# Optimization experiments

Hardware: AMD Instinct MI355X
Metric: run time of the kernel (lower is better)

The kernel has to match this reference:

```python
import jax, jax.numpy as jnp
import numpy as np

NEG_SLOPE = 0.2  # PyG GATConv default leaky_relu slope
EPS = 1e-16


def layer_norm(x, g, b):
    mu = x.mean(-1, keepdims=True)
    var = ((x - mu) ** 2).mean(-1, keepdims=True)
    return (x - mu) * jax.lax.rsqrt(var + 1e-5) * g + b


def gat_conv(x, src, dst, n, W, a_src, a_dst, bias):
    # x: [N, C_in]; W: [C_in, H*C]; a_src/a_dst: [H, C]; concat=False -> mean over heads
    H, C = a_src.shape
    xh = (x @ W).reshape(n, H, C)                      # [N, H, C]
    s_src = jnp.einsum('nhc,hc->nh', xh, a_src)         # [N, H]
    s_dst = jnp.einsum('nhc,hc->nh', xh, a_dst)         # [N, H]
    e = jax.nn.leaky_relu(s_src[src] + s_dst[dst], NEG_SLOPE)  # [E, H]
    # segment softmax over incoming edges of each destination node
    m = jax.ops.segment_max(e, dst, num_segments=n)     # [N, H]
    ee = jnp.exp(e - m[dst])
    z = jax.ops.segment_sum(ee, dst, num_segments=n)    # [N, H]
    alpha = ee / (z[dst] + EPS)                         # [E, H]
    msg = xh[src] * alpha[:, :, None]                   # [E, H, C]
    out = jax.ops.segment_sum(msg, dst, num_segments=n) # [N, H, C]
    return out.mean(axis=1) + bias                      # [N, C]


def setup_inputs() -> dict:
    key = jax.random.key(0)
    N, E, C, H, L = 50000, 400000, 64, 4, 2
    ks = jax.random.split(key, 16)
    x = jax.random.normal(ks[0], (N, C), dtype=jnp.float32)
    edge_index = jax.random.randint(ks[1], (2, E), 0, N, dtype=jnp.int64)
    sc = 1.0 / np.sqrt(C)
    return {
        'x': x,
        'edge_index': edge_index,
        'Wg': jax.random.normal(ks[2], (L, C, H * C), dtype=jnp.float32) * sc,
        'att_src': jax.random.normal(ks[3], (L, H, C), dtype=jnp.float32) * sc,
        'att_dst': jax.random.normal(ks[4], (L, H, C), dtype=jnp.float32) * sc,
        'att_bias': jnp.zeros((L, C), dtype=jnp.float32),
        'ln1_g': jnp.ones((L, C), dtype=jnp.float32),
        'ln1_b': jnp.zeros((L, C), dtype=jnp.float32),
        'W1': jax.random.normal(ks[5], (L, C, C), dtype=jnp.float32) * sc,
        'b1': jnp.zeros((L, C), dtype=jnp.float32),
        'W2': jax.random.normal(ks[6], (L, C, C), dtype=jnp.float32) * sc,
        'b2': jnp.zeros((L, C), dtype=jnp.float32),
        'ln2_g': jnp.ones((L, C), dtype=jnp.float32),
        'ln2_b': jnp.zeros((L, C), dtype=jnp.float32),
    }


def reference(x, edge_index, Wg, att_src, att_dst, att_bias,
              ln1_g, ln1_b, W1, b1, W2, b2, ln2_g, ln2_b):
    n = x.shape[0]
    L = Wg.shape[0]
    # PyG GATConv adds self loops by default
    loops = jnp.arange(n, dtype=edge_index.dtype)
    src = jnp.concatenate([edge_index[0], loops])
    dst = jnp.concatenate([edge_index[1], loops])
    for i in range(L):
        x_att = gat_conv(x, src, dst, n, Wg[i], att_src[i], att_dst[i], att_bias[i])
        x = layer_norm(x + x_att, ln1_g[i], ln1_b[i])
        h = jax.nn.relu(x @ W1[i] + b1[i])
        h = h @ W2[i] + b2[i]
        x = layer_norm(x + h, ln2_g[i], ln2_b[i])
    return x
```

## Files before the change

kernel.cpp:

```cpp
#include <hip/hip_runtime.h>
#include <hip/hip_bf16.h>
#include <float.h>

#define C 64
#define H 4
#define HC 256
#define NEG_SLOPE 0.2f
#define EPS_SEG 1e-16f
#define LN_EPS 1e-5f
#define ROWB 576

typedef __attribute__((ext_vector_type(8))) short bf16x8;
typedef __attribute__((ext_vector_type(4))) float f32x4;

__device__ __forceinline__ float warp_sum(float v) {
#pragma unroll
    for (int m = 32; m >= 1; m >>= 1) v += __shfl_xor(v, m, 64);
    return v;
}

__device__ __forceinline__ unsigned short f2bf(float f) {
    unsigned int u = __float_as_uint(f);
    return (unsigned short)((u + 0x7FFF + ((u >> 16) & 1)) >> 16);
}
__device__ __forceinline__ float bf2f(unsigned short u) {
    return __uint_as_float(((unsigned int)u) << 16);
}


__global__ void k_zero(int* __restrict__ a, int n) {
    int i = blockIdx.x * blockDim.x + threadIdx.x;
    int stride = gridDim.x * blockDim.x;
    for (int j = i; j < n; j += stride) a[j] = 0;
}

__global__ void k_count(const int* __restrict__ ei, int* __restrict__ counts,
                        int E, int Etot) {
    int eid = blockIdx.x * blockDim.x + threadIdx.x;
    if (eid >= Etot) return;
    int d = (eid < E) ? ei[E + eid] : eid - E;
    atomicAdd(&counts[d], 1);
}

__global__ __launch_bounds__(256) void k_scan1(const int* __restrict__ counts,
                                               int* __restrict__ tmp,
                                               int* __restrict__ bsum, int N) {
    __shared__ int sm[256];
    int t = threadIdx.x;
    int i = blockIdx.x * 256 + t;
    sm[t] = (i < N) ? counts[i] : 0;
    __syncthreads();
    for (int off = 1; off < 256; off <<= 1) {
        int add = (t >= off) ? sm[t - off] : 0;
        __syncthreads();
        sm[t] += add;
        __syncthreads();
    }
    if (i < N) tmp[i] = sm[t];
    if (t == 255) bsum[blockIdx.x] = sm[255];
}

__global__ __launch_bounds__(256) void k_scan2(int* __restrict__ bsum, int nb) {
    __shared__ int sm[256];
    int t = threadIdx.x;
    sm[t] = (t < nb) ? bsum[t] : 0;
    __syncthreads();
    for (int off = 1; off < 256; off <<= 1) {
        int add = (t >= off) ? sm[t - off] : 0;
        __syncthreads();
        sm[t] += add;
        __syncthreads();
    }
    if (t < nb) bsum[t] = (t > 0) ? sm[t - 1] : 0;
}

__global__ __launch_bounds__(256) void k_scan3(const int* __restrict__ tmp,
                                               const int* __restrict__ boff,
                                               int* __restrict__ rowptr,
                                               int* __restrict__ cursor, int N) {
    int i = blockIdx.x * 256 + threadIdx.x;
    if (i < N) {
        rowptr[i + 1] = tmp[i] + boff[blockIdx.x];
        cursor[i] = 0;
    }
    if (i == 0) rowptr[0] = 0;
}

__global__ void k_fill(const int* __restrict__ ei, const int* __restrict__ rowptr,
                       int* __restrict__ cursor, int* __restrict__ col,
                       int E, int Etot) {
    int eid = blockIdx.x * blockDim.x + threadIdx.x;
    if (eid >= Etot) return;
    int s, d;
    if (eid < E) { s = ei[eid]; d = ei[E + eid]; } else { s = d = eid - E; }
    int pos = rowptr[d] + atomicAdd(&cursor[d], 1);
    col[pos] = s;
}


__global__ void k_prep_x(const float4* __restrict__ xin, ushort4* __restrict__ xb,
                         int n4, int npad4) {
    int i = blockIdx.x * blockDim.x + threadIdx.x;
    int st = gridDim.x * blockDim.x;
    for (int j = i; j < npad4; j += st) {
        ushort4 o;
        if (j < n4) {
            float4 v = xin[j];
            o.x = f2bf(v.x); o.y = f2bf(v.y); o.z = f2bf(v.z); o.w = f2bf(v.w);
        } else {
            o.x = o.y = o.z = o.w = 0;
        }
        xb[j] = o;
    }
}

__global__ void k_prep_weights(const float* __restrict__ Wg,
                               const float* __restrict__ W1, const float* __restrict__ W2,
                               unsigned short* __restrict__ Wgt,
                               unsigned short* __restrict__ W1t,
                               unsigned short* __restrict__ W2t, int L) {
    int i = blockIdx.x * 256 + threadIdx.x;
    int nWg = L * C * HC;
    int nW = L * C * C;
    if (i < nWg) {
        int l = i / (C * HC);
        int r = i - l * C * HC;
        int n = r >> 6, k = r & 63;
        Wgt[(size_t)l * HC * C + n * C + k] = f2bf(Wg[(size_t)l * C * HC + k * HC + n]);
    } else if (i < nWg + nW) {
        int j = i - nWg;
        int l = j / (C * C);
        int r = j - l * C * C;
        int n = r >> 6, k = r & 63;
        W1t[(size_t)l * C * C + n * C + k] = f2bf(W1[(size_t)l * C * C + k * C + n]);
        W2t[(size_t)l * C * C + n * C + k] = f2bf(W2[(size_t)l * C * C + k * C + n]);
    }
}

__global__ __launch_bounds__(256) void k_gemm_mfma(
    const unsigned short* __restrict__ xb, const unsigned short* __restrict__ Wgt,
    const float* __restrict__ a_src, const float* __restrict__ a_dst,
    char* __restrict__ xhs, float* __restrict__ s_dst, int N)
{
    int w = threadIdx.x >> 6, l = threadIdx.x & 63;
    int n0 = blockIdx.x * 64;
    int lr = l & 15, lk = (l >> 4) * 8;
    bf16x8 bfr[4][2];
    float as[4], ad[4];
#pragma unroll
    for (int ct = 0; ct < 4; ct++) {
        int colg = w * 64 + ct * 16 + lr;
#pragma unroll
        for (int ks = 0; ks < 2; ks++)
            bfr[ct][ks] = *reinterpret_cast<const bf16x8*>(Wgt + colg * C + ks * 32 + lk);
        as[ct] = a_src[w * C + ct * 16 + lr];
        ad[ct] = a_dst[w * C + ct * 16 + lr];
    }
#pragma unroll
    for (int rt = 0; rt < 4; rt++) {
        const unsigned short* arow = xb + (size_t)(n0 + rt * 16 + lr) * C + lk;
        bf16x8 a0 = *reinterpret_cast<const bf16x8*>(arow);
        bf16x8 a1 = *reinterpret_cast<const bf16x8*>(arow + 32);
        f32x4 acc[4];
#pragma unroll
        for (int ct = 0; ct < 4; ct++) {
            acc[ct] = (f32x4){0.f, 0.f, 0.f, 0.f};
            acc[ct] = __builtin_amdgcn_mfma_f32_16x16x32_bf16(a0, bfr[ct][0], acc[ct], 0, 0, 0);
            acc[ct] = __builtin_amdgcn_mfma_f32_16x16x32_bf16(a1, bfr[ct][1], acc[ct], 0, 0, 0);
        }
        int nbase = n0 + rt * 16 + (l >> 4) * 4;
#pragma unroll
        for (int ct = 0; ct < 4; ct++) {
            int cb = (w * 64 + ct * 16 + lr) * 2;
#pragma unroll
            for (int r = 0; r < 4; r++) {
                int n = nbase + r;
                if (n < N)
                    *(unsigned short*)(xhs + (size_t)n * ROWB + cb) = f2bf(acc[ct][r]);
            }
        }
#pragma unroll
        for (int r = 0; r < 4; r++) {
            float ps = acc[0][r] * as[0] + acc[1][r] * as[1]
                     + acc[2][r] * as[2] + acc[3][r] * as[3];
            float pd = acc[0][r] * ad[0] + acc[1][r] * ad[1]
                     + acc[2][r] * ad[2] + acc[3][r] * ad[3];
#pragma unroll
            for (int off = 1; off < 16; off <<= 1) {
                ps += __shfl_xor(ps, off, 64);
                pd += __shfl_xor(pd, off, 64);
            }
            int n = nbase + r;
            if (lr == 0 && n < N) {
                *(float*)(xhs + (size_t)n * ROWB + 512 + w * 4) = ps;
                s_dst[n * H + w] = pd;
            }
        }
    }
}

__global__ __launch_bounds__(256) void k_gat_node(
    const int* __restrict__ rowptr, const int* __restrict__ col,
    const float* __restrict__ s_dst, const char* __restrict__ xhs,
    const float* __restrict__ x_in, const float* __restrict__ bias,
    const float* __restrict__ g, const float* __restrict__ b,
    float* __restrict__ x1, unsigned short* __restrict__ x1b, int N)
{
    int n = (blockIdx.x * blockDim.x + threadIdx.x) >> 6;
    int l = threadIdx.x & 63;
    int h = l >> 4, gq = l & 15;
    if (n >= N) return;
    int r0 = rowptr[n], r1 = rowptr[n + 1];

    float4 xi = *(const float4*)(x_in + (size_t)n * C + gq * 4);
    float4 bia = *(const float4*)(bias + gq * 4);
    float sdh = s_dst[n * H + h];

    int laneoff = h * 128 + gq * 8;
    int ssoff = 512 + h * 4;

    float a0 = 0.f, a1 = 0.f, a2 = 0.f, a3 = 0.f, z = 0.f;

    int j = r0;
    for (; j + 4 <= r1; j += 4) {
        int s0 = col[j], s1 = col[j + 1], s2 = col[j + 2], s3 = col[j + 3];
        const char* p0 = xhs + (size_t)s0 * ROWB;
        const char* p1 = xhs + (size_t)s1 * ROWB;
        const char* p2 = xhs + (size_t)s2 * ROWB;
        const char* p3 = xhs + (size_t)s3 * ROWB;
        uint2 v0 = *(const uint2*)(p0 + laneoff);
        uint2 v1 = *(const uint2*)(p1 + laneoff);
        uint2 v2 = *(const uint2*)(p2 + laneoff);
        uint2 v3 = *(const uint2*)(p3 + laneoff);
        float e0 = *(const float*)(p0 + ssoff) + sdh;
        float e1 = *(const float*)(p1 + ssoff) + sdh;
        float e2 = *(const float*)(p2 + ssoff) + sdh;
        float e3 = *(const float*)(p3 + ssoff) + sdh;
        float w0 = __expf(fmaxf(e0, NEG_SLOPE * e0));
        float w1 = __expf(fmaxf(e1, NEG_SLOPE * e1));
        float w2 = __expf(fmaxf(e2, NEG_SLOPE * e2));
        float w3 = __expf(fmaxf(e3, NEG_SLOPE * e3));
        a0 += w0 * __uint_as_float(v0.x << 16);
        a1 += w0 * __uint_as_float(v0.x & 0xFFFF0000u);
        a2 += w0 * __uint_as_float(v0.y << 16);
        a3 += w0 * __uint_as_float(v0.y & 0xFFFF0000u);
        a0 += w1 * __uint_as_float(v1.x << 16);
        a1 += w1 * __uint_as_float(v1.x & 0xFFFF0000u);
        a2 += w1 * __uint_as_float(v1.y << 16);
        a3 += w1 * __uint_as_float(v1.y & 0xFFFF0000u);
        a0 += w2 * __uint_as_float(v2.x << 16);
        a1 += w2 * __uint_as_float(v2.x & 0xFFFF0000u);
        a2 += w2 * __uint_as_float(v2.y << 16);
        a3 += w2 * __uint_as_float(v2.y & 0xFFFF0000u);
        a0 += w3 * __uint_as_float(v3.x << 16);
        a1 += w3 * __uint_as_float(v3.x & 0xFFFF0000u);
        a2 += w3 * __uint_as_float(v3.y << 16);
        a3 += w3 * __uint_as_float(v3.y & 0xFFFF0000u);
        z += w0 + w1 + w2 + w3;
    }
    {
        int t = r1 - j;
        int s0 = 0, s1 = 0, s2 = 0;
        if (t > 0) s0 = col[j];
        if (t > 1) s1 = col[j + 1];
        if (t > 2) s2 = col[j + 2];
        const char* p0 = xhs + (size_t)s0 * ROWB;
        const char* p1 = xhs + (size_t)s1 * ROWB;
        const char* p2 = xhs + (size_t)s2 * ROWB;
        uint2 v0 = {0, 0}, v1 = {0, 0}, v2 = {0, 0};
        float e0 = 0.f, e1 = 0.f, e2 = 0.f;
        if (t > 0) { v0 = *(const uint2*)(p0 + laneoff); e0 = *(const float*)(p0 + ssoff) + sdh; }
        if (t > 1) { v1 = *(const uint2*)(p1 + laneoff); e1 = *(const float*)(p1 + ssoff) + sdh; }
        if (t > 2) { v2 = *(const uint2*)(p2 + laneoff); e2 = *(const float*)(p2 + ssoff) + sdh; }
        float w0 = (t > 0) ? __expf(fmaxf(e0, NEG_SLOPE * e0)) : 0.f;
        float w1 = (t > 1) ? __expf(fmaxf(e1, NEG_SLOPE * e1)) : 0.f;
        float w2 = (t > 2) ? __expf(fmaxf(e2, NEG_SLOPE * e2)) : 0.f;
        a0 += w0 * __uint_as_float(v0.x << 16);
        a1 += w0 * __uint_as_float(v0.x & 0xFFFF0000u);
        a2 += w0 * __uint_as_float(v0.y << 16);
        a3 += w0 * __uint_as_float(v0.y & 0xFFFF0000u);
        a0 += w1 * __uint_as_float(v1.x << 16);
        a1 += w1 * __uint_as_float(v1.x & 0xFFFF0000u);
        a2 += w1 * __uint_as_float(v1.y << 16);
        a3 += w1 * __uint_as_float(v1.y & 0xFFFF0000u);
        a0 += w2 * __uint_as_float(v2.x << 16);
        a1 += w2 * __uint_as_float(v2.x & 0xFFFF0000u);
        a2 += w2 * __uint_as_float(v2.y << 16);
        a3 += w2 * __uint_as_float(v2.y & 0xFFFF0000u);
        z += w0 + w1 + w2;
    }

    float inv = 0.25f / (z + EPS_SEG);
    a0 *= inv; a1 *= inv; a2 *= inv; a3 *= inv;
#pragma unroll
    for (int off = 16; off <= 32; off <<= 1) {
        a0 += __shfl_xor(a0, off, 64);
        a1 += __shfl_xor(a1, off, 64);
        a2 += __shfl_xor(a2, off, 64);
        a3 += __shfl_xor(a3, off, 64);
    }
    float y0 = xi.x + a0 + bia.x;
    float y1 = xi.y + a1 + bia.y;
    float y2 = xi.z + a2 + bia.z;
    float y3 = xi.w + a3 + bia.w;
    float mu = warp_sum(y0 + y1 + y2 + y3) * (1.f / (C * 4));
    float d0 = y0 - mu, d1 = y1 - mu, d2 = y2 - mu, d3 = y3 - mu;
    float var = warp_sum(d0 * d0 + d1 * d1 + d2 * d2 + d3 * d3) * (1.f / (C * 4));
    float rs = rsqrtf(var + LN_EPS);
    if (h == 0) {
        float4 gg = *(const float4*)(g + gq * 4);
        float4 bb = *(const float4*)(b + gq * 4);
        float4 o;
        o.x = d0 * rs * gg.x + bb.x;
        o.y = d1 * rs * gg.y + bb.y;
        o.z = d2 * rs * gg.z + bb.z;
        o.w = d3 * rs * gg.w + bb.w;
        *(float4*)(x1 + (size_t)n * C + gq * 4) = o;
        ushort4 ob;
        ob.x = f2bf(o.x); ob.y = f2bf(o.y); ob.z = f2bf(o.z); ob.w = f2bf(o.w);
        *(ushort4*)(x1b + (size_t)n * C + gq * 4) = ob;
    }
}

__global__ __launch_bounds__(256) void k_ffn_mfma(
    const float* __restrict__ x1f, const unsigned short* __restrict__ x1b,
    const unsigned short* __restrict__ W1t, const unsigned short* __restrict__ W2t,
    const float* __restrict__ b1, const float* __restrict__ b2,
    const float* __restrict__ g, const float* __restrict__ b,
    float* __restrict__ xout, unsigned short* __restrict__ xb, int N)
{
    __shared__ unsigned short hls[64 * 64];
    int w = threadIdx.x >> 6, l = threadIdx.x & 63;
    int lr = l & 15, q = l >> 4, lk = q * 8;
    int n0 = blockIdx.x * 64;

    {
        bf16x8 bf[4][2];
#pragma unroll
        for (int ct = 0; ct < 4; ct++)
#pragma unroll
            for (int ks = 0; ks < 2; ks++)
                bf[ct][ks] = *reinterpret_cast<const bf16x8*>(
                    W1t + (ct * 16 + lr) * C + ks * 32 + lk);
        const unsigned short* arow = x1b + (size_t)(n0 + w * 16 + lr) * C + lk;
        bf16x8 a0 = *reinterpret_cast<const bf16x8*>(arow);
        bf16x8 a1 = *reinterpret_cast<const bf16x8*>(arow + 32);
        f32x4 acc[4];
#pragma unroll
        for (int ct = 0; ct < 4; ct++) {
            acc[ct] = (f32x4){0.f, 0.f, 0.f, 0.f};
            acc[ct] = __builtin_amdgcn_mfma_f32_16x16x32_bf16(a0, bf[ct][0], acc[ct], 0, 0, 0);
            acc[ct] = __builtin_amdgcn_mfma_f32_16x16x32_bf16(a1, bf[ct][1], acc[ct], 0, 0, 0);
        }
#pragma unroll
        for (int ct = 0; ct < 4; ct++) {
            float bc = b1[ct * 16 + lr];
#pragma unroll
            for (int r = 0; r < 4; r++) {
                float v = fmaxf(acc[ct][r] + bc, 0.f);
                int rowb = w * 16 + q * 4 + r;
                int byte = rowb * 128 + (ct * 16 + lr) * 2;
                byte ^= (rowb & 7) << 4;
                *(unsigned short*)((char*)hls + byte) = f2bf(v);
            }
        }
    }
    __syncthreads();

    bf16x8 bf[4][2];
#pragma unroll
    for (int ct = 0; ct < 4; ct++)
#pragma unroll
        for (int ks = 0; ks < 2; ks++)
            bf[ct][ks] = *reinterpret_cast<const bf16x8*>(
                W2t + (ct * 16 + lr) * C + ks * 32 + lk);
    bf16x8 h0, h1;
    {
        int rowb = w * 16 + lr;
        int swz = (rowb & 7) << 4;
        int byte0 = (rowb * 128 + q * 16) ^ swz;
        int byte1 = (rowb * 128 + 64 + q * 16) ^ swz;
        h0 = *(bf16x8*)((char*)hls + byte0);
        h1 = *(bf16x8*)((char*)hls + byte1);
    }
    f32x4 acc[4];
#pragma unroll
    for (int ct = 0; ct < 4; ct++) {
        acc[ct] = (f32x4){0.f, 0.f, 0.f, 0.f};
        acc[ct] = __builtin_amdgcn_mfma_f32_16x16x32_bf16(h0, bf[ct][0], acc[ct], 0, 0, 0);
        acc[ct] = __builtin_amdgcn_mfma_f32_16x16x32_bf16(h1, bf[ct][1], acc[ct], 0, 0, 0);
    }

    float b2c[4], gc[4], bc[4];
#pragma unroll
    for (int ct = 0; ct < 4; ct++) {
        int cg = ct * 16 + lr;
        b2c[ct] = b2[cg]; gc[ct] = g[cg]; bc[ct] = b[cg];
    }
    float yv[4][4];
#pragma unroll
    for (int r = 0; r < 4; r++) {
        int n = n0 + w * 16 + q * 4 + r;
        bool ok = n < N;
#pragma unroll
        for (int ct = 0; ct < 4; ct++) {
            float xr = ok ? x1f[(size_t)n * C + ct * 16 + lr] : 0.f;
            yv[ct][r] = acc[ct][r] + b2c[ct] + xr;
        }
    }
#pragma unroll
    for (int r = 0; r < 4; r++) {
        int n = n0 + w * 16 + q * 4 + r;
        float s = yv[0][r] + yv[1][r] + yv[2][r] + yv[3][r];
#pragma unroll
        for (int off = 1; off < 16; off <<= 1) s += __shfl_xor(s, off, 64);
        float mu = s * (1.f / C);
        float d0 = yv[0][r] - mu, d1 = yv[1][r] - mu;
        float d2 = yv[2][r] - mu, d3 = yv[3][r] - mu;
        float vs = d0 * d0 + d1 * d1 + d2 * d2 + d3 * d3;
#pragma unroll
        for (int off = 1; off < 16; off <<= 1) vs += __shfl_xor(vs, off, 64);
        float rs = rsqrtf(vs * (1.f / C) + LN_EPS);
        if (n < N) {
            float dd[4] = {d0, d1, d2, d3};
#pragma unroll
            for (int ct = 0; ct < 4; ct++) {
                float o = dd[ct] * rs * gc[ct] + bc[ct];
                xout[(size_t)n * C + ct * 16 + lr] = o;
                xb[(size_t)n * C + ct * 16 + lr] = f2bf(o);
            }
        }
    }
}

extern "C" void kernel_launch(void* const* d_in, const int* in_sizes, int n_in,
                              void* d_out, int out_size, void* d_ws, size_t ws_size,
                              hipStream_t stream) {
    const float* x        = (const float*)d_in[0];
    const int*   ei       = (const int*)d_in[1];
    const float* Wg       = (const float*)d_in[2];
    const float* a_src    = (const float*)d_in[3];
    const float* a_dst    = (const float*)d_in[4];
    const float* att_bias = (const float*)d_in[5];
    const float* ln1_g    = (const float*)d_in[6];
    const float* ln1_b    = (const float*)d_in[7];
    const float* W1       = (const float*)d_in[8];
    const float* b1       = (const float*)d_in[9];
    const float* W2       = (const float*)d_in[10];
    const float* b2       = (const float*)d_in[11];
    const float* ln2_g    = (const float*)d_in[12];
    const float* ln2_b    = (const float*)d_in[13];
    float* xout = (float*)d_out;

    int N = in_sizes[0] / C;
    int E = in_sizes[1] / 2;
    int Etot = E + N;
    int L = in_sizes[2] / (C * HC);
    int nb = (N + 255) / 256;
    int Npad = (N + 63) & ~63;

    char* p = (char*)d_ws;
    auto alloc = [&](size_t bytes) { void* r = (void*)p; p += (bytes + 255) & ~(size_t)255; return r; };
    float* s_dst = (float*)alloc((size_t)N * H * 4);
    float* x1    = (float*)alloc((size_t)N * C * 4);
    int* rowptr  = (int*)alloc((size_t)(N + 1) * 4);
    int* col     = (int*)alloc((size_t)Etot * 4);
    int* counts  = (int*)alloc((size_t)N * 4);
    int* tmp     = (int*)alloc((size_t)N * 4);
    int* bsum    = (int*)alloc((size_t)nb * 4);
    unsigned short* xb  = (unsigned short*)alloc((size_t)Npad * C * 2);
    unsigned short* x1b = (unsigned short*)alloc((size_t)Npad * C * 2);
    unsigned short* Wgt = (unsigned short*)alloc((size_t)L * HC * C * 2);
    unsigned short* W1t = (unsigned short*)alloc((size_t)L * C * C * 2);
    unsigned short* W2t = (unsigned short*)alloc((size_t)L * C * C * 2);
    char* xhs = (char*)alloc((size_t)N * ROWB);

    k_zero<<<256, 256, 0, stream>>>(counts, N);
    k_count<<<(Etot + 255) / 256, 256, 0, stream>>>(ei, counts, E, Etot);
    k_scan1<<<nb, 256, 0, stream>>>(counts, tmp, bsum, N);
    k_scan2<<<1, 256, 0, stream>>>(bsum, nb);
    k_scan3<<<nb, 256, 0, stream>>>(tmp, bsum, rowptr, counts, N);
    k_fill<<<(Etot + 255) / 256, 256, 0, stream>>>(ei, rowptr, counts, col, E, Etot);
    k_prep_x<<<2048, 256, 0, stream>>>((const float4*)x, (ushort4*)xb,
                                       N * C / 4, Npad * C / 4);
    {
        int tot = L * C * HC + L * C * C;
        k_prep_weights<<<(tot + 255) / 256, 256, 0, stream>>>(Wg, W1, W2, Wgt, W1t, W2t, L);
    }

    for (int l = 0; l < L; l++) {
        const float* xin = (l == 0) ? x : xout;
        k_gemm_mfma<<<Npad / 64, 256, 0, stream>>>(
            xb, Wgt + (size_t)l * HC * C, a_src + l * H * C, a_dst + l * H * C,
            xhs, s_dst, N);
        k_gat_node<<<(N + 3) / 4, 256, 0, stream>>>(
            rowptr, col, s_dst, xhs, xin,
            att_bias + l * C, ln1_g + l * C, ln1_b + l * C, x1, x1b, N);
        k_ffn_mfma<<<Npad / 64, 256, 0, stream>>>(
            x1, x1b, W1t + (size_t)l * C * C, W2t + (size_t)l * C * C,
            b1 + l * C, b2 + l * C, ln2_g + l * C, ln2_b + l * C, xout, xb, N);
    }
}
```

Before: 218.5 us.

## Map 16 lanes per node in GAT aggregation with double-buffered neighbor loads

The GAT aggregation kernel now gives each destination node 16 lanes instead of a full 64-lane wavefront, so one wavefront serves four nodes. Each lane handles two heads and 8 channels using 16-byte loads. The neighbor loop is software-pipelined: the next neighbor's row is fetched while the current one is accumulated. The aim is to raise the number of gather loads in flight per wavefront and cut idle lanes. In exchange, the four nodes in a wavefront diverge by degree because the loop runs until all are done, and each lane uses more registers.

After: 225.3 us. 1.03x slower.

```diff
diff --git a/kernel.cpp b/kernel.cpp
--- a/kernel.cpp
+++ b/kernel.cpp
@@ -22,9 +22,6 @@
 __device__ __forceinline__ unsigned short f2bf(float f) {
     unsigned int u = __float_as_uint(f);
     return (unsigned short)((u + 0x7FFF + ((u >> 16) & 1)) >> 16);
-}
-__device__ __forceinline__ float bf2f(unsigned short u) {
-    return __uint_as_float(((unsigned int)u) << 16);
 }
 
 
@@ -206,119 +203,126 @@
     const float* __restrict__ g, const float* __restrict__ b,
     float* __restrict__ x1, unsigned short* __restrict__ x1b, int N)
 {
-    int n = (blockIdx.x * blockDim.x + threadIdx.x) >> 6;
     int l = threadIdx.x & 63;
-    int h = l >> 4, gq = l & 15;
-    if (n >= N) return;
-    int r0 = rowptr[n], r1 = rowptr[n + 1];
-
-    float4 xi = *(const float4*)(x_in + (size_t)n * C + gq * 4);
-    float4 bia = *(const float4*)(bias + gq * 4);
-    float sdh = s_dst[n * H + h];
-
-    int laneoff = h * 128 + gq * 8;
-    int ssoff = 512 + h * 4;
-
-    float a0 = 0.f, a1 = 0.f, a2 = 0.f, a3 = 0.f, z = 0.f;
-
-    int j = r0;
-    for (; j + 4 <= r1; j += 4) {
-        int s0 = col[j], s1 = col[j + 1], s2 = col[j + 2], s3 = col[j + 3];
-        const char* p0 = xhs + (size_t)s0 * ROWB;
-        const char* p1 = xhs + (size_t)s1 * ROWB;
-        const char* p2 = xhs + (size_t)s2 * ROWB;
-        const char* p3 = xhs + (size_t)s3 * ROWB;
-        uint2 v0 = *(const uint2*)(p0 + laneoff);
-        uint2 v1 = *(const uint2*)(p1 + laneoff);
-        uint2 v2 = *(const uint2*)(p2 + laneoff);
-        uint2 v3 = *(const uint2*)(p3 + laneoff);
-        float e0 = *(const float*)(p0 + ssoff) + sdh;
-        float e1 = *(const float*)(p1 + ssoff) + sdh;
-        float e2 = *(const float*)(p2 + ssoff) + sdh;
-        float e3 = *(const float*)(p3 + ssoff) + sdh;
-        float w0 = __expf(fmaxf(e0, NEG_SLOPE * e0));
-        float w1 = __expf(fmaxf(e1, NEG_SLOPE * e1));
-        float w2 = __expf(fmaxf(e2, NEG_SLOPE * e2));
-        float w3 = __expf(fmaxf(e3, NEG_SLOPE * e3));
-        a0 += w0 * __uint_as_float(v0.x << 16);
-        a1 += w0 * __uint_as_float(v0.x & 0xFFFF0000u);
-        a2 += w0 * __uint_as_float(v0.y << 16);
-        a3 += w0 * __uint_as_float(v0.y & 0xFFFF0000u);
-        a0 += w1 * __uint_as_float(v1.x << 16);
-        a1 += w1 * __uint_as_float(v1.x & 0xFFFF0000u);
-        a2 += w1 * __uint_as_float(v1.y << 16);
-        a3 += w1 * __uint_as_float(v1.y & 0xFFFF0000u);
-        a0 += w2 * __uint_as_float(v2.x << 16);
-        a1 += w2 * __uint_as_float(v2.x & 0xFFFF0000u);
-        a2 += w2 * __uint_as_float(v2.y << 16);
-        a3 += w2 * __uint_as_float(v2.y & 0xFFFF0000u);
-        a0 += w3 * __uint_as_float(v3.x << 16);
-        a1 += w3 * __uint_as_float(v3.x & 0xFFFF0000u);
-        a2 += w3 * __uint_as_float(v3.y << 16);
-        a3 += w3 * __uint_as_float(v3.y & 0xFFFF0000u);
-        z += w0 + w1 + w2 + w3;
-    }
-    {
-        int t = r1 - j;
-        int s0 = 0, s1 = 0, s2 = 0;
-        if (t > 0) s0 = col[j];
-        if (t > 1) s1 = col[j + 1];
-        if (t > 2) s2 = col[j + 2];
-        const char* p0 = xhs + (size_t)s0 * ROWB;
-        const char* p1 = xhs + (size_t)s1 * ROWB;
-        const char* p2 = xhs + (size_t)s2 * ROWB;
-        uint2 v0 = {0, 0}, v1 = {0, 0}, v2 = {0, 0};
-        float e0 = 0.f, e1 = 0.f, e2 = 0.f;
-        if (t > 0) { v0 = *(const uint2*)(p0 + laneoff); e0 = *(const float*)(p0 + ssoff) + sdh; }
-        if (t > 1) { v1 = *(const uint2*)(p1 + laneoff); e1 = *(const float*)(p1 + ssoff) + sdh; }
-        if (t > 2) { v2 = *(const uint2*)(p2 + laneoff); e2 = *(const float*)(p2 + ssoff) + sdh; }
-        float w0 = (t > 0) ? __expf(fmaxf(e0, NEG_SLOPE * e0)) : 0.f;
-        float w1 = (t > 1) ? __expf(fmaxf(e1, NEG_SLOPE * e1)) : 0.f;
-        float w2 = (t > 2) ? __expf(fmaxf(e2, NEG_SLOPE * e2)) : 0.f;
-        a0 += w0 * __uint_as_float(v0.x << 16);
-        a1 += w0 * __uint_as_float(v0.x & 0xFFFF0000u);
-        a2 += w0 * __uint_as_float(v0.y << 16);
-        a3 += w0 * __uint_as_float(v0.y & 0xFFFF0000u);
-        a0 += w1 * __uint_as_float(v1.x << 16);
-        a1 += w1 * __uint_as_float(v1.x & 0xFFFF0000u);
-        a2 += w1 * __uint_as_float(v1.y << 16);
-        a3 += w1 * __uint_as_float(v1.y & 0xFFFF0000u);
-        a0 += w2 * __uint_as_float(v2.x << 16);
-        a1 += w2 * __uint_as_float(v2.x & 0xFFFF0000u);
-        a2 += w2 * __uint_as_float(v2.y << 16);
-        a3 += w2 * __uint_as_float(v2.y & 0xFFFF0000u);
-        z += w0 + w1 + w2;
-    }
-
-    float inv = 0.25f / (z + EPS_SEG);
-    a0 *= inv; a1 *= inv; a2 *= inv; a3 *= inv;
-#pragma unroll
-    for (int off = 16; off <= 32; off <<= 1) {
-        a0 += __shfl_xor(a0, off, 64);
-        a1 += __shfl_xor(a1, off, 64);
-        a2 += __shfl_xor(a2, off, 64);
-        a3 += __shfl_xor(a3, off, 64);
-    }
-    float y0 = xi.x + a0 + bia.x;
-    float y1 = xi.y + a1 + bia.y;
-    float y2 = xi.z + a2 + bia.z;
-    float y3 = xi.w + a3 + bia.w;
-    float mu = warp_sum(y0 + y1 + y2 + y3) * (1.f / (C * 4));
-    float d0 = y0 - mu, d1 = y1 - mu, d2 = y2 - mu, d3 = y3 - mu;
-    float var = warp_sum(d0 * d0 + d1 * d1 + d2 * d2 + d3 * d3) * (1.f / (C * 4));
-    float rs = rsqrtf(var + LN_EPS);
-    if (h == 0) {
-        float4 gg = *(const float4*)(g + gq * 4);
-        float4 bb = *(const float4*)(b + gq * 4);
-        float4 o;
-        o.x = d0 * rs * gg.x + bb.x;
-        o.y = d1 * rs * gg.y + bb.y;
-        o.z = d2 * rs * gg.z + bb.z;
-        o.w = d3 * rs * gg.w + bb.w;
-        *(float4*)(x1 + (size_t)n * C + gq * 4) = o;
-        ushort4 ob;
-        ob.x = f2bf(o.x); ob.y = f2bf(o.y); ob.z = f2bf(o.z); ob.w = f2bf(o.w);
-        *(ushort4*)(x1b + (size_t)n * C + gq * 4) = ob;
+    int il = l & 15;
+    int n = blockIdx.x * 16 + ((threadIdx.x >> 6) << 2) + (l >> 4);
+    bool nvalid = n < N;
+    int nn = nvalid ? n : 0;
+    int r0 = rowptr[nn];
+    int r1 = rowptr[nn + 1];
+    int deg = nvalid ? (r1 - r0) : 0;
+
+    int hsel = (il >> 3) & 1;
+    float sdA = s_dst[nn * H + hsel];
+    float sdB = s_dst[nn * H + 2 + hsel];
+    int c0 = (il & 7) * 8;
+    int byteoff = il * 16;
+
+    float acc0[8], acc1[8];
+#pragma unroll
+    for (int k = 0; k < 8; k++) { acc0[k] = 0.f; acc1[k] = 0.f; }
+    float zA = 0.f, zB = 0.f;
+
+    uint4 a0v = {0,0,0,0}, a1v = {0,0,0,0};
+    float4 asv = {0.f,0.f,0.f,0.f};
+    bool actA = 0 < deg;
+    if (actA) {
+        const char* p = xhs + (size_t)col[r0] * ROWB;
+        a0v = *(const uint4*)(p + byteoff);
+        a1v = *(const uint4*)(p + 256 + byteoff);
+        asv = *(const float4*)(p + 512);
+    }
+
+#define GAT_COMPUTE(V0, V1, SV, ACT)                                          \
+    {                                                                         \
+        float ea = (hsel ? (SV).y : (SV).x) + sdA;                            \
+        float eb = (hsel ? (SV).w : (SV).z) + sdB;                            \
+        float wA = (ACT) ? __expf(fmaxf(ea, NEG_SLOPE * ea)) : 0.f;           \
+        float wB = (ACT) ? __expf(fmaxf(eb, NEG_SLOPE * eb)) : 0.f;           \
+        unsigned int uu0[4] = {(V0).x, (V0).y, (V0).z, (V0).w};               \
+        unsigned int uu1[4] = {(V1).x, (V1).y, (V1).z, (V1).w};               \
+        _Pragma("unroll")                                                     \
+        for (int q = 0; q < 4; q++) {                                         \
+            acc0[2*q]   += wA * __uint_as_float(uu0[q] << 16);                \
+            acc0[2*q+1] += wA * __uint_as_float(uu0[q] & 0xFFFF0000u);        \
+            acc1[2*q]   += wB * __uint_as_float(uu1[q] << 16);                \
+            acc1[2*q+1] += wB * __uint_as_float(uu1[q] & 0xFFFF0000u);        \
+        }                                                                     \
+        zA += wA; zB += wB;                                                   \
+    }
+
+    int t = 0;
+    while (__any(actA)) {
+        bool actB = (t + 1) < deg;
+        uint4 b0v = {0,0,0,0}, b1v = {0,0,0,0};
+        float4 bsv = {0.f,0.f,0.f,0.f};
+        if (actB) {
+            const char* p = xhs + (size_t)col[r0 + t + 1] * ROWB;
+            b0v = *(const uint4*)(p + byteoff);
+            b1v = *(const uint4*)(p + 256 + byteoff);
+            bsv = *(const float4*)(p + 512);
+        }
+        GAT_COMPUTE(a0v, a1v, asv, actA);
+        actA = (t + 2) < deg;
+        if (actA) {
+            const char* p = xhs + (size_t)col[r0 + t + 2] * ROWB;
+            a0v = *(const uint4*)(p + byteoff);
+            a1v = *(const uint4*)(p + 256 + byteoff);
+            asv = *(const float4*)(p + 512);
+        } else {
+            a0v = (uint4){0,0,0,0}; a1v = (uint4){0,0,0,0};
+            asv = (float4){0.f,0.f,0.f,0.f};
+        }
+        GAT_COMPUTE(b0v, b1v, bsv, actB);
+        t += 2;
+    }
+#undef GAT_COMPUTE
+
+    float izA = 1.f / (zA + EPS_SEG);
+    float izB = 1.f / (zB + EPS_SEG);
+    float y[8];
+#pragma unroll
+    for (int k = 0; k < 8; k++) {
+        float v = acc0[k] * izA + acc1[k] * izB;
+        v += __shfl_xor(v, 8, 64);
+        y[k] = v * 0.25f;
+    }
+    float xi[8], bi[8];
+    *(float4*)&xi[0] = *(const float4*)(x_in + (size_t)nn * C + c0);
+    *(float4*)&xi[4] = *(const float4*)(x_in + (size_t)nn * C + c0 + 4);
+    *(float4*)&bi[0] = *(const float4*)(bias + c0);
+    *(float4*)&bi[4] = *(const float4*)(bias + c0 + 4);
+#pragma unroll
+    for (int k = 0; k < 8; k++) y[k] += xi[k] + bi[k];
+    float s = 0.f;
+#pragma unroll
+    for (int k = 0; k < 8; k++) s += y[k];
+#pragma unroll
+    for (int off = 1; off <= 8; off <<= 1) s += __shfl_xor(s, off, 64);
+    float mu = s * (1.f / 128.f);
+    float vs = 0.f;
+    float dv[8];
+#pragma unroll
+    for (int k = 0; k < 8; k++) { dv[k] = y[k] - mu; vs += dv[k] * dv[k]; }
+#pragma unroll
+    for (int off = 1; off <= 8; off <<= 1) vs += __shfl_xor(vs, off, 64);
+    float rs = rsqrtf(vs * (1.f / 128.f) + LN_EPS);
+    if (il < 8 && nvalid) {
+        float gg[8], bb[8];
+        *(float4*)&gg[0] = *(const float4*)(g + c0);
+        *(float4*)&gg[4] = *(const float4*)(g + c0 + 4);
+        *(float4*)&bb[0] = *(const float4*)(b + c0);
+        *(float4*)&bb[4] = *(const float4*)(b + c0 + 4);
+        float o[8];
+        ushort4 ob0, ob1;
+#pragma unroll
+        for (int k = 0; k < 8; k++) o[k] = dv[k] * rs * gg[k] + bb[k];
+        *(float4*)(x1 + (size_t)n * C + c0) = *(float4*)&o[0];
+        *(float4*)(x1 + (size_t)n * C + c0 + 4) = *(float4*)&o[4];
+        ob0.x = f2bf(o[0]); ob0.y = f2bf(o[1]); ob0.z = f2bf(o[2]); ob0.w = f2bf(o[3]);
+        ob1.x = f2bf(o[4]); ob1.y = f2bf(o[5]); ob1.z = f2bf(o[6]); ob1.w = f2bf(o[7]);
+        *(ushort4*)(x1b + (size_t)n * C + c0) = ob0;
+        *(ushort4*)(x1b + (size_t)n * C + c0 + 4) = ob1;
     }
 }
 
@@ -493,7 +497,7 @@
         k_gemm_mfma<<<Npad / 64, 256, 0, stream>>>(
             xb, Wgt + (size_t)l * HC * C, a_src + l * H * C, a_dst + l * H * C,
             xhs, s_dst, N);
-        k_gat_node<<<(N + 3) / 4, 256, 0, stream>>>(
+        k_gat_node<<<(N + 15) / 16, 256, 0, stream>>>(
             rowptr, col, s_dst, xhs, xin,
             att_bias + l * C, ln1_g + l * C, ln1_b + l * C, x1, x1b, N);
         k_ffn_mfma<<<Npad / 64, 256, 0, stream>>>(
```

## Split s_src out of packed node rows and unroll edge gather by eight

Applied to the files above, without the earlier changes.

The packed per-node row that stored bf16 features plus the source attention scores (576 bytes) is split into a 512-byte feature array and a separate compact s_src array. The GAT aggregation loop is unrolled from four to eight edges per iteration, with a tail that handles up to seven remaining edges. The aim is power-of-two row strides and more outstanding gather loads per wavefront to hide latency. The cost is an extra scattered load stream for s_src per edge and higher register pressure from the wider unroll.

After: 234.3 us. 1.07x slower.

```diff
diff --git a/kernel.cpp b/kernel.cpp
--- a/kernel.cpp
+++ b/kernel.cpp
@@ -8,7 +8,6 @@
 #define NEG_SLOPE 0.2f
 #define EPS_SEG 1e-16f
 #define LN_EPS 1e-5f
-#define ROWB 576
 
 typedef __attribute__((ext_vector_type(8))) short bf16x8;
 typedef __attribute__((ext_vector_type(4))) float f32x4;
@@ -22,9 +21,6 @@
 __device__ __forceinline__ unsigned short f2bf(float f) {
     unsigned int u = __float_as_uint(f);
     return (unsigned short)((u + 0x7FFF + ((u >> 16) & 1)) >> 16);
-}
-__device__ __forceinline__ float bf2f(unsigned short u) {
-    return __uint_as_float(((unsigned int)u) << 16);
 }
 
 
@@ -140,7 +136,8 @@
 __global__ __launch_bounds__(256) void k_gemm_mfma(
     const unsigned short* __restrict__ xb, const unsigned short* __restrict__ Wgt,
     const float* __restrict__ a_src, const float* __restrict__ a_dst,
-    char* __restrict__ xhs, float* __restrict__ s_dst, int N)
+    unsigned short* __restrict__ xh, float* __restrict__ s_src,
+    float* __restrict__ s_dst, int N)
 {
     int w = threadIdx.x >> 6, l = threadIdx.x & 63;
     int n0 = blockIdx.x * 64;
@@ -171,12 +168,11 @@
         int nbase = n0 + rt * 16 + (l >> 4) * 4;
 #pragma unroll
         for (int ct = 0; ct < 4; ct++) {
-            int cb = (w * 64 + ct * 16 + lr) * 2;
+            int colg = w * 64 + ct * 16 + lr;
 #pragma unroll
             for (int r = 0; r < 4; r++) {
                 int n = nbase + r;
-                if (n < N)
-                    *(unsigned short*)(xhs + (size_t)n * ROWB + cb) = f2bf(acc[ct][r]);
+                if (n < N) xh[(size_t)n * HC + colg] = f2bf(acc[ct][r]);
             }
         }
 #pragma unroll
@@ -192,7 +188,7 @@
             }
             int n = nbase + r;
             if (lr == 0 && n < N) {
-                *(float*)(xhs + (size_t)n * ROWB + 512 + w * 4) = ps;
+                s_src[n * H + w] = ps;
                 s_dst[n * H + w] = pd;
             }
         }
@@ -201,7 +197,8 @@
 
 __global__ __launch_bounds__(256) void k_gat_node(
     const int* __restrict__ rowptr, const int* __restrict__ col,
-    const float* __restrict__ s_dst, const char* __restrict__ xhs,
+    const float* __restrict__ s_src, const float* __restrict__ s_dst,
+    const unsigned short* __restrict__ xh,
     const float* __restrict__ x_in, const float* __restrict__ bias,
     const float* __restrict__ g, const float* __restrict__ b,
     float* __restrict__ x1, unsigned short* __restrict__ x1b, int N)
@@ -216,79 +213,79 @@
     float4 bia = *(const float4*)(bias + gq * 4);
     float sdh = s_dst[n * H + h];
 
+    const char* xbase = (const char*)xh;
     int laneoff = h * 128 + gq * 8;
-    int ssoff = 512 + h * 4;
 
     float a0 = 0.f, a1 = 0.f, a2 = 0.f, a3 = 0.f, z = 0.f;
 
+#define GACC(vv, ww)                                         \
+    a0 += (ww) * __uint_as_float((vv).x << 16);              \
+    a1 += (ww) * __uint_as_float((vv).x & 0xFFFF0000u);      \
+    a2 += (ww) * __uint_as_float((vv).y << 16);              \
+    a3 += (ww) * __uint_as_float((vv).y & 0xFFFF0000u);      \
+    z += (ww);
+
     int j = r0;
-    for (; j + 4 <= r1; j += 4) {
-        int s0 = col[j], s1 = col[j + 1], s2 = col[j + 2], s3 = col[j + 3];
-        const char* p0 = xhs + (size_t)s0 * ROWB;
-        const char* p1 = xhs + (size_t)s1 * ROWB;
-        const char* p2 = xhs + (size_t)s2 * ROWB;
-        const char* p3 = xhs + (size_t)s3 * ROWB;
-        uint2 v0 = *(const uint2*)(p0 + laneoff);
-        uint2 v1 = *(const uint2*)(p1 + laneoff);
-        uint2 v2 = *(const uint2*)(p2 + laneoff);
-        uint2 v3 = *(const uint2*)(p3 + laneoff);
-        float e0 = *(const float*)(p0 + ssoff) + sdh;
-        float e1 = *(const float*)(p1 + ssoff) + sdh;
-        float e2 = *(const float*)(p2 + ssoff) + sdh;
-        float e3 = *(const float*)(p3 + ssoff) + sdh;
+    for (; j + 8 <= r1; j += 8) {
+        int s0 = col[j],     s1 = col[j + 1], s2 = col[j + 2], s3 = col[j + 3];
+        int s4 = col[j + 4], s5 = col[j + 5], s6 = col[j + 6], s7 = col[j + 7];
+        uint2 v0 = *(const uint2*)(xbase + (size_t)s0 * 512 + laneoff);
+        uint2 v1 = *(const uint2*)(xbase + (size_t)s1 * 512 + laneoff);
+        uint2 v2 = *(const uint2*)(xbase + (size_t)s2 * 512 + laneoff);
+        uint2 v3 = *(const uint2*)(xbase + (size_t)s3 * 512 + laneoff);
+        uint2 v4 = *(const uint2*)(xbase + (size_t)s4 * 512 + laneoff);
+        uint2 v5 = *(const uint2*)(xbase + (size_t)s5 * 512 + laneoff);
+        uint2 v6 = *(const uint2*)(xbase + (size_t)s6 * 512 + laneoff);
+        uint2 v7 = *(const uint2*)(xbase + (size_t)s7 * 512 + laneoff);
+        float e0 = s_src[s0 * H + h] + sdh;
+        float e1 = s_src[s1 * H + h] + sdh;
+        float e2 = s_src[s2 * H + h] + sdh;
+        float e3 = s_src[s3 * H + h] + sdh;
+        float e4 = s_src[s4 * H + h] + sdh;
+        float e5 = s_src[s5 * H + h] + sdh;
+        float e6 = s_src[s6 * H + h] + sdh;
+        float e7 = s_src[s7 * H + h] + sdh;
         float w0 = __expf(fmaxf(e0, NEG_SLOPE * e0));
         float w1 = __expf(fmaxf(e1, NEG_SLOPE * e1));
         float w2 = __expf(fmaxf(e2, NEG_SLOPE * e2));
         float w3 = __expf(fmaxf(e3, NEG_SLOPE * e3));
-        a0 += w0 * __uint_as_float(v0.x << 16);
-        a1 += w0 * __uint_as_float(v0.x & 0xFFFF0000u);
-        a2 += w0 * __uint_as_float(v0.y << 16);
-        a3 += w0 * __uint_as_float(v0.y & 0xFFFF0000u);
-        a0 += w1 * __uint_as_float(v1.x << 16);
-        a1 += w1 * __uint_as_float(v1.x & 0xFFFF0000u);
-        a2 += w1 * __uint_as_float(v1.y << 16);
-        a3 += w1 * __uint_as_float(v1.y & 0xFFFF0000u);
-        a0 += w2 * __uint_as_float(v2.x << 16);
-        a1 += w2 * __uint_as_float(v2.x & 0xFFFF0000u);
-        a2 += w2 * __uint_as_float(v2.y << 16);
-        a3 += w2 * __uint_as_float(v2.y & 0xFFFF0000u);
-        a0 += w3 * __uint_as_float(v3.x << 16);
-        a1 += w3 * __uint_as_float(v3.x & 0xFFFF0000u);
-        a2 += w3 * __uint_as_float(v3.y << 16);
-        a3 += w3 * __uint_as_float(v3.y & 0xFFFF0000u);
-        z += w0 + w1 + w2 + w3;
-    }
-    {
-        int t = r1 - j;
-        int s0 = 0, s1 = 0, s2 = 0;
+        float w4 = __expf(fmaxf(e4, NEG_SLOPE * e4));
+        float w5 = __expf(fmaxf(e5, NEG_SLOPE * e5));
+        float w6 = __expf(fmaxf(e6, NEG_SLOPE * e6));
+        float w7 = __expf(fmaxf(e7, NEG_SLOPE * e7));
+        GACC(v0, w0) GACC(v1, w1) GACC(v2, w2) GACC(v3, w3)
+        GACC(v4, w4) GACC(v5, w5) GACC(v6, w6) GACC(v7, w7)
+    }
+    int t = r1 - j;
+    if (t) {
+        int s0 = 0, s1 = 0, s2 = 0, s3 = 0, s4 = 0, s5 = 0, s6 = 0;
         if (t > 0) s0 = col[j];
         if (t > 1) s1 = col[j + 1];
         if (t > 2) s2 = col[j + 2];
-        const char* p0 = xhs + (size_t)s0 * ROWB;
-        const char* p1 = xhs + (size_t)s1 * ROWB;
-        const char* p2 = xhs + (size_t)s2 * ROWB;
-        uint2 v0 = {0, 0}, v1 = {0, 0}, v2 = {0, 0};
-        float e0 = 0.f, e1 = 0.f, e2 = 0.f;
-        if (t > 0) { v0 = *(const uint2*)(p0 + laneoff); e0 = *(const float*)(p0 + ssoff) + sdh; }
-        if (t > 1) { v1 = *(const uint2*)(p1 + laneoff); e1 = *(const float*)(p1 + ssoff) + sdh; }
-        if (t > 2) { v2 = *(const uint2*)(p2 + laneoff); e2 = *(const float*)(p2 + ssoff) + sdh; }
+        if (t > 3) s3 = col[j + 3];
+        if (t > 4) s4 = col[j + 4];
+        if (t > 5) s5 = col[j + 5];
+        if (t > 6) s6 = col[j + 6];
+        uint2 v0 = {0,0}, v1 = {0,0}, v2 = {0,0}, v3 = {0,0}, v4 = {0,0}, v5 = {0,0}, v6 = {0,0};
+        float e0 = 0.f, e1 = 0.f, e2 = 0.f, e3 = 0.f, e4 = 0.f, e5 = 0.f, e6 = 0.f;
+        if (t > 0) { v0 = *(const uint2*)(xbase + (size_t)s0 * 512 + laneoff); e0 = s_src[s0 * H + h] + sdh; }
+        if (t > 1) { v1 = *(const uint2*)(xbase + (size_t)s1 * 512 + laneoff); e1 = s_src[s1 * H + h] + sdh; }
+        if (t > 2) { v2 = *(const uint2*)(xbase + (size_t)s2 * 512 + laneoff); e2 = s_src[s2 * H + h] + sdh; }
+        if (t > 3) { v3 = *(const uint2*)(xbase + (size_t)s3 * 512 + laneoff); e3 = s_src[s3 * H + h] + sdh; }
+        if (t > 4) { v4 = *(const uint2*)(xbase + (size_t)s4 * 512 + laneoff); e4 = s_src[s4 * H + h] + sdh; }
+        if (t > 5) { v5 = *(const uint2*)(xbase + (size_t)s5 * 512 + laneoff); e5 = s_src[s5 * H + h] + sdh; }
+        if (t > 6) { v6 = *(const uint2*)(xbase + (size_t)s6 * 512 + laneoff); e6 = s_src[s6 * H + h] + sdh; }
         float w0 = (t > 0) ? __expf(fmaxf(e0, NEG_SLOPE * e0)) : 0.f;
         float w1 = (t > 1) ? __expf(fmaxf(e1, NEG_SLOPE * e1)) : 0.f;
         float w2 = (t > 2) ? __expf(fmaxf(e2, NEG_SLOPE * e2)) : 0.f;
-        a0 += w0 * __uint_as_float(v0.x << 16);
-        a1 += w0 * __uint_as_float(v0.x & 0xFFFF0000u);
-        a2 += w0 * __uint_as_float(v0.y << 16);
-        a3 += w0 * __uint_as_float(v0.y & 0xFFFF0000u);
-        a0 += w1 * __uint_as_float(v1.x << 16);
-        a1 += w1 * __uint_as_float(v1.x & 0xFFFF0000u);
-        a2 += w1 * __uint_as_float(v1.y << 16);
-        a3 += w1 * __uint_as_float(v1.y & 0xFFFF0000u);
-        a0 += w2 * __uint_as_float(v2.x << 16);
-        a1 += w2 * __uint_as_float(v2.x & 0xFFFF0000u);
-        a2 += w2 * __uint_as_float(v2.y << 16);
-        a3 += w2 * __uint_as_float(v2.y & 0xFFFF0000u);
-        z += w0 + w1 + w2;
-    }
+        float w3 = (t > 3) ? __expf(fmaxf(e3, NEG_SLOPE * e3)) : 0.f;
+        float w4 = (t > 4) ? __expf(fmaxf(e4, NEG_SLOPE * e4)) : 0.f;
+        float w5 = (t > 5) ? __expf(fmaxf(e5, NEG_SLOPE * e5)) : 0.f;
+        float w6 = (t > 6) ? __expf(fmaxf(e6, NEG_SLOPE * e6)) : 0.f;
+        GACC(v0, w0) GACC(v1, w1) GACC(v2, w2) GACC(v3, w3)
+        GACC(v4, w4) GACC(v5, w5) GACC(v6, w6)
+    }
+#undef GACC
 
     float inv = 0.25f / (z + EPS_SEG);
     a0 *= inv; a1 *= inv; a2 *= inv; a3 *= inv;
@@ -461,6 +458,7 @@
 
     char* p = (char*)d_ws;
     auto alloc = [&](size_t bytes) { void* r = (void*)p; p += (bytes + 255) & ~(size_t)255; return r; };
+    float* s_src = (float*)alloc((size_t)N * H * 4);
     float* s_dst = (float*)alloc((size_t)N * H * 4);
     float* x1    = (float*)alloc((size_t)N * C * 4);
     int* rowptr  = (int*)alloc((size_t)(N + 1) * 4);
@@ -473,7 +471,7 @@
     unsigned short* Wgt = (unsigned short*)alloc((size_t)L * HC * C * 2);
     unsigned short* W1t = (unsigned short*)alloc((size_t)L * C * C * 2);
     unsigned short* W2t = (unsigned short*)alloc((size_t)L * C * C * 2);
-    char* xhs = (char*)alloc((size_t)N * ROWB);
+    unsigned short* xh  = (unsigned short*)alloc((size_t)N * HC * 2);
 
     k_zero<<<256, 256, 0, stream>>>(counts, N);
     k_count<<<(Etot + 255) / 256, 256, 0, stream>>>(ei, counts, E, Etot);
@@ -492,9 +490,9 @@
         const float* xin = (l == 0) ? x : xout;
         k_gemm_mfma<<<Npad / 64, 256, 0, stream>>>(
             xb, Wgt + (size_t)l * HC * C, a_src + l * H * C, a_dst + l * H * C,
-            xhs, s_dst, N);
+            xh, s_src, s_dst, N);
         k_gat_node<<<(N + 3) / 4, 256, 0, stream>>>(
-            rowptr, col, s_dst, xhs, xin,
+            rowptr, col, s_src, s_dst, xh, xin,
             att_bias + l * C, ln1_g + l * C, ln1_b + l * C, x1, x1b, N);
         k_ffn_mfma<<<Npad / 64, 256, 0, stream>>>(
             x1, x1b, W1t + (size_t)l * C * C, W2t + (size_t)l * C * C,
```

## Split s_src out of projected rows and stage GEMM output through LDS

Applied to the files above, without the earlier changes.

The projected features become a dense 512-byte-per-row bf16 array, and the source attention scores move to a separate s_src array instead of being packed into 576-byte rows. The GEMM kernel now writes its bf16 output into an LDS tile and copies it out with coalesced 16-byte stores, replacing scattered 2-byte global stores. The gather kernel then reads aligned 512-byte rows plus a small s_src array that is more likely to stay in cache. In exchange the GEMM uses about 33KB of LDS per block plus a barrier, and the gather issues a separate s_src load for each edge.

Measured after the change: 212.3 us. 1.03x faster.

```diff
diff --git a/kernel.cpp b/kernel.cpp
--- a/kernel.cpp
+++ b/kernel.cpp
@@ -8,7 +8,7 @@
 #define NEG_SLOPE 0.2f
 #define EPS_SEG 1e-16f
 #define LN_EPS 1e-5f
-#define ROWB 576
+#define LDSP 528
 
 typedef __attribute__((ext_vector_type(8))) short bf16x8;
 typedef __attribute__((ext_vector_type(4))) float f32x4;
@@ -22,9 +22,6 @@
 __device__ __forceinline__ unsigned short f2bf(float f) {
     unsigned int u = __float_as_uint(f);
     return (unsigned short)((u + 0x7FFF + ((u >> 16) & 1)) >> 16);
-}
-__device__ __forceinline__ float bf2f(unsigned short u) {
-    return __uint_as_float(((unsigned int)u) << 16);
 }
 
 
@@ -140,11 +137,13 @@
 __global__ __launch_bounds__(256) void k_gemm_mfma(
     const unsigned short* __restrict__ xb, const unsigned short* __restrict__ Wgt,
     const float* __restrict__ a_src, const float* __restrict__ a_dst,
-    char* __restrict__ xhs, float* __restrict__ s_dst, int N)
+    unsigned short* __restrict__ xh, float* __restrict__ s_src,
+    float* __restrict__ s_dst, int N)
 {
+    __shared__ char tile[64 * LDSP];
     int w = threadIdx.x >> 6, l = threadIdx.x & 63;
     int n0 = blockIdx.x * 64;
-    int lr = l & 15, lk = (l >> 4) * 8;
+    int lr = l & 15, q = l >> 4, lk = q * 8;
     bf16x8 bfr[4][2];
     float as[4], ad[4];
 #pragma unroll
@@ -168,16 +167,13 @@
             acc[ct] = __builtin_amdgcn_mfma_f32_16x16x32_bf16(a0, bfr[ct][0], acc[ct], 0, 0, 0);
             acc[ct] = __builtin_amdgcn_mfma_f32_16x16x32_bf16(a1, bfr[ct][1], acc[ct], 0, 0, 0);
         }
-        int nbase = n0 + rt * 16 + (l >> 4) * 4;
+        int rowl = rt * 16 + q * 4;
 #pragma unroll
         for (int ct = 0; ct < 4; ct++) {
             int cb = (w * 64 + ct * 16 + lr) * 2;
 #pragma unroll
-            for (int r = 0; r < 4; r++) {
-                int n = nbase + r;
-                if (n < N)
-                    *(unsigned short*)(xhs + (size_t)n * ROWB + cb) = f2bf(acc[ct][r]);
-            }
+            for (int r = 0; r < 4; r++)
+                *(unsigned short*)(tile + (rowl + r) * LDSP + cb) = f2bf(acc[ct][r]);
         }
 #pragma unroll
         for (int r = 0; r < 4; r++) {
@@ -190,18 +186,28 @@
                 ps += __shfl_xor(ps, off, 64);
                 pd += __shfl_xor(pd, off, 64);
             }
-            int n = nbase + r;
-            if (lr == 0 && n < N) {
-                *(float*)(xhs + (size_t)n * ROWB + 512 + w * 4) = ps;
-                s_dst[n * H + w] = pd;
+            if (lr == 0) {
+                int n = n0 + rowl + r;
+                s_src[(size_t)n * H + w] = ps;
+                s_dst[(size_t)n * H + w] = pd;
             }
         }
+    }
+    __syncthreads();
+#pragma unroll
+    for (int it = 0; it < 8; it++) {
+        int off = threadIdx.x * 16 + it * 4096;
+        int row = off >> 9;
+        int cin = off & 511;
+        uint4 v = *(const uint4*)(tile + row * LDSP + cin);
+        *(uint4*)((char*)xh + (size_t)(n0 + row) * 512 + cin) = v;
     }
 }
 
 __global__ __launch_bounds__(256) void k_gat_node(
     const int* __restrict__ rowptr, const int* __restrict__ col,
-    const float* __restrict__ s_dst, const char* __restrict__ xhs,
+    const float* __restrict__ s_src, const float* __restrict__ s_dst,
+    const unsigned short* __restrict__ xh,
     const float* __restrict__ x_in, const float* __restrict__ bias,
     const float* __restrict__ g, const float* __restrict__ b,
     float* __restrict__ x1, unsigned short* __restrict__ x1b, int N)
@@ -216,26 +222,22 @@
     float4 bia = *(const float4*)(bias + gq * 4);
     float sdh = s_dst[n * H + h];
 
+    const char* xbase = (const char*)xh;
     int laneoff = h * 128 + gq * 8;
-    int ssoff = 512 + h * 4;
 
     float a0 = 0.f, a1 = 0.f, a2 = 0.f, a3 = 0.f, z = 0.f;
 
     int j = r0;
     for (; j + 4 <= r1; j += 4) {
         int s0 = col[j], s1 = col[j + 1], s2 = col[j + 2], s3 = col[j + 3];
-        const char* p0 = xhs + (size_t)s0 * ROWB;
-        const char* p1 = xhs + (size_t)s1 * ROWB;
-        const char* p2 = xhs + (size_t)s2 * ROWB;
-        const char* p3 = xhs + (size_t)s3 * ROWB;
-        uint2 v0 = *(const uint2*)(p0 + laneoff);
-        uint2 v1 = *(const uint2*)(p1 + laneoff);
-        uint2 v2 = *(const uint2*)(p2 + laneoff);
-        uint2 v3 = *(const uint2*)(p3 + laneoff);
-        float e0 = *(const float*)(p0 + ssoff) + sdh;
-        float e1 = *(const float*)(p1 + ssoff) + sdh;
-        float e2 = *(const float*)(p2 + ssoff) + sdh;
-        float e3 = *(const float*)(p3 + ssoff) + sdh;
+        uint2 v0 = *(const uint2*)(xbase + (size_t)s0 * 512 + laneoff);
+        uint2 v1 = *(const uint2*)(xbase + (size_t)s1 * 512 + laneoff);
+        uint2 v2 = *(const uint2*)(xbase + (size_t)s2 * 512 + laneoff);
+        uint2 v3 = *(const uint2*)(xbase + (size_t)s3 * 512 + laneoff);
+        float e0 = s_src[s0 * H + h] + sdh;
+        float e1 = s_src[s1 * H + h] + sdh;
+        float e2 = s_src[s2 * H + h] + sdh;
+        float e3 = s_src[s3 * H + h] + sdh;
         float w0 = __expf(fmaxf(e0, NEG_SLOPE * e0));
         float w1 = __expf(fmaxf(e1, NEG_SLOPE * e1));
         float w2 = __expf(fmaxf(e2, NEG_SLOPE * e2));
@@ -264,14 +266,11 @@
         if (t > 0) s0 = col[j];
         if (t > 1) s1 = col[j + 1];
         if (t > 2) s2 = col[j + 2];
-        const char* p0 = xhs + (size_t)s0 * ROWB;
-        const char* p1 = xhs + (size_t)s1 * ROWB;
-        const char* p2 = xhs + (size_t)s2 * ROWB;
         uint2 v0 = {0, 0}, v1 = {0, 0}, v2 = {0, 0};
         float e0 = 0.f, e1 = 0.f, e2 = 0.f;
-        if (t > 0) { v0 = *(const uint2*)(p0 + laneoff); e0 = *(const float*)(p0 + ssoff) + sdh; }
-        if (t > 1) { v1 = *(const uint2*)(p1 + laneoff); e1 = *(const float*)(p1 + ssoff) + sdh; }
-        if (t > 2) { v2 = *(const uint2*)(p2 + laneoff); e2 = *(const float*)(p2 + ssoff) + sdh; }
+        if (t > 0) { v0 = *(const uint2*)(xbase + (size_t)s0 * 512 + laneoff); e0 = s_src[s0 * H + h] + sdh; }
+        if (t > 1) { v1 = *(const uint2*)(xbase + (size_t)s1 * 512 + laneoff); e1 = s_src[s1 * H + h] + sdh; }
+        if (t > 2) { v2 = *(const uint2*)(xbase + (size_t)s2 * 512 + laneoff); e2 = s_src[s2 * H + h] + sdh; }
         float w0 = (t > 0) ? __expf(fmaxf(e0, NEG_SLOPE * e0)) : 0.f;
         float w1 = (t > 1) ? __expf(fmaxf(e1, NEG_SLOPE * e1)) : 0.f;
         float w2 = (t > 2) ? __expf(fmaxf(e2, NEG_SLOPE * e2)) : 0.f;
@@ -461,7 +460,8 @@
 
     char* p = (char*)d_ws;
     auto alloc = [&](size_t bytes) { void* r = (void*)p; p += (bytes + 255) & ~(size_t)255; return r; };
-    float* s_dst = (float*)alloc((size_t)N * H * 4);
+    float* s_src = (float*)alloc((size_t)Npad * H * 4);
+    float* s_dst = (float*)alloc((size_t)Npad * H * 4);
     float* x1    = (float*)alloc((size_t)N * C * 4);
     int* rowptr  = (int*)alloc((size_t)(N + 1) * 4);
     int* col     = (int*)alloc((size_t)Etot * 4);
@@ -473,7 +473,7 @@
     unsigned short* Wgt = (unsigned short*)alloc((size_t)L * HC * C * 2);
     unsigned short* W1t = (unsigned short*)alloc((size_t)L * C * C * 2);
     unsigned short* W2t = (unsigned short*)alloc((size_t)L * C * C * 2);
-    char* xhs = (char*)alloc((size_t)N * ROWB);
+    unsigned short* xh  = (unsigned short*)alloc((size_t)Npad * HC * 2);
 
     k_zero<<<256, 256, 0, stream>>>(counts, N);
     k_count<<<(Etot + 255) / 256, 256, 0, stream>>>(ei, counts, E, Etot);
@@ -492,9 +492,9 @@
         const float* xin = (l == 0) ? x : xout;
         k_gemm_mfma<<<Npad / 64, 256, 0, stream>>>(
             xb, Wgt + (size_t)l * HC * C, a_src + l * H * C, a_dst + l * H * C,
-            xhs, s_dst, N);
+            xh, s_src, s_dst, N);
         k_gat_node<<<(N + 3) / 4, 256, 0, stream>>>(
-            rowptr, col, s_dst, xhs, xin,
+            rowptr, col, s_src, s_dst, xh, xin,
             att_bias + l * C, ln1_g + l * C, ln1_b + l * C, x1, x1b, N);
         k_ffn_mfma<<<Npad / 64, 256, 0, stream>>>(
             x1, x1b, W1t + (size_t)l * C * C, W2t + (size_t)l * C * C,
```
